# Kernel tuning notes

Measured on AMD Instinct MI355X. Metric: run time of the kernel, lower is better.

The kernel has to match this reference:

```python
import jax, jax.numpy as jnp
import numpy as np

NUM_USERS = 50000
NUM_ITEMS = 50000
LATENT_DIM = 64
NUM_INTERACTIONS = 1600000
N_LAYERS = 4  # 4 ODE blocks, euler 1-step each == 4 LightGCN propagations


def setup_inputs() -> dict:
    key = jax.random.key(0)
    k1, k2, k3, k4, k5 = jax.random.split(key, 5)
    user_emb = 0.1 * jax.random.normal(k1, (NUM_USERS, LATENT_DIM), dtype=jnp.float32)
    item_emb = 0.1 * jax.random.normal(k2, (NUM_ITEMS, LATENT_DIM), dtype=jnp.float32)
    eu = jax.random.randint(k3, (NUM_INTERACTIONS,), 0, NUM_USERS, dtype=jnp.int32)
    ei = jax.random.randint(jax.random.fold_in(k3, 1), (NUM_INTERACTIONS,), 0, NUM_ITEMS, dtype=jnp.int32)
    edge_index = jnp.stack([eu, ei])  # [2, E] user->item interactions
    users = jax.random.randint(k4, (4096,), 0, NUM_USERS, dtype=jnp.int32)
    items = jax.random.randint(k5, (4096,), 0, NUM_ITEMS, dtype=jnp.int32)
    return {"user_emb": user_emb, "item_emb": item_emb,
            "edge_index": edge_index, "users": users, "items": items}


def _graph(edge_index):
    # Symmetric bipartite graph over n_users + n_items nodes, normalized D^-1/2 A D^-1/2.
    eu, ei = edge_index[0], edge_index[1] + NUM_USERS
    rows = jnp.concatenate([eu, ei])
    cols = jnp.concatenate([ei, eu])
    n = NUM_USERS + NUM_ITEMS
    deg = jax.ops.segment_sum(jnp.ones_like(rows, dtype=jnp.float32), rows, num_segments=n)
    dinv = jnp.where(deg > 0, jax.lax.rsqrt(jnp.maximum(deg, 1.0)), 0.0)
    w = dinv[rows] * dinv[cols]  # [2E]
    return rows, cols, w


def _propagate(x, rows, cols, w):
    # sparse matmul: out[r] += w_e * x[c]  (irregular gather + segment-sum)
    n = NUM_USERS + NUM_ITEMS
    return jax.ops.segment_sum(x[cols] * w[:, None], rows, num_segments=n)


def _computer(user_emb, item_emb, edge_index):
    rows, cols, w = _graph(edge_index)
    e0 = jnp.concatenate([user_emb, item_emb])  # [N, d]
    # fixed-time euler: block_k(x) = x + A x; residual subtraction leaves A x
    embs = [e0]
    x = e0
    for _ in range(N_LAYERS):
        x = _propagate(x, rows, cols, w)
        embs.append(x)
    light_out = jnp.mean(jnp.stack(embs, axis=1), axis=1)  # [N, d]
    return light_out[:NUM_USERS], light_out[NUM_USERS:]


def reference(user_emb, item_emb, edge_index, users, items):
    all_users, all_items = _computer(user_emb, item_emb, edge_index)
    u = all_users[users]
    i = all_items[items]
    gamma = jnp.sum(u * i, axis=1)  # [B]
    return gamma
```

## Files before the change

kernel.cpp:

```cpp
#include <hip/hip_runtime.h>

#define LAT 64
#define ELLC 64
#define RB 256
#define RBSH 8
#define MAXBUK 512
#define RPT 8

#define SC0 64.0f
#define RSC 3.0f

typedef float f32x2 __attribute__((ext_vector_type(2)));

__global__ void __launch_bounds__(1024)
bin_k(const int* __restrict__ eu, const int* __restrict__ ei,
      int* __restrict__ gcur, unsigned int* __restrict__ bbuf,
      int2* __restrict__ ovf, int* __restrict__ ovfc,
      int E, int U, int nbuk, int cap, int ovf_cap) {
    __shared__ int lcnt[MAXBUK];
    __shared__ int lbase[MAXBUK];
    for (int i = threadIdx.x; i < nbuk; i += blockDim.x) lcnt[i] = 0;
    __syncthreads();
    int tid = blockIdx.x * blockDim.x + threadIdx.x;
    int stride = gridDim.x * blockDim.x;
    int ru[RPT], rc[RPT];
    int ne = 0;
#pragma unroll
    for (int k = 0; k < RPT; ++k) {
        int d = tid + k * stride;
        if (d < E) {
            int u = eu[d], c = ei[d] + U;
            ru[k] = u; rc[k] = c; ne = k + 1;
            atomicAdd(&lcnt[u >> RBSH], 1);
            atomicAdd(&lcnt[c >> RBSH], 1);
        }
    }
    __syncthreads();
    for (int b = threadIdx.x; b < nbuk; b += blockDim.x)
        lbase[b] = atomicAdd(&gcur[b], lcnt[b]);
    __syncthreads();
#pragma unroll
    for (int k = 0; k < RPT; ++k) {
        if (k < ne) {
            int u = ru[k], c = rc[k];
            int b = u >> RBSH;
            int pos = atomicAdd(&lbase[b], 1);
            if (pos < cap)
                bbuf[(size_t)b * cap + pos] = ((unsigned)(u & (RB - 1)) << 17) | (unsigned)c;
            else { int o = atomicAdd(ovfc, 1); if (o < ovf_cap) ovf[o] = make_int2(u, c); }
            b = c >> RBSH;
            pos = atomicAdd(&lbase[b], 1);
            if (pos < cap)
                bbuf[(size_t)b * cap + pos] = ((unsigned)(c & (RB - 1)) << 17) | (unsigned)u;
            else { int o = atomicAdd(ovfc, 1); if (o < ovf_cap) ovf[o] = make_int2(c, u); }
        }
    }
}

__global__ void __launch_bounds__(1024)
build_k(const unsigned int* __restrict__ bbuf, const int* __restrict__ gcur,
        int* __restrict__ cnt, int* __restrict__ colE, float* __restrict__ dinv,
        const float* __restrict__ ue, const float* __restrict__ ie,
        unsigned char* __restrict__ y0,
        int2* __restrict__ rovf, int* __restrict__ rovfc,
        int N, int U, int cap, int rovf_cap) {
    __shared__ int lcnt[RB];
    __shared__ float ldv[RB];
    int b = blockIdx.x;
    for (int i = threadIdx.x; i < RB; i += blockDim.x) lcnt[i] = 0;
    __syncthreads();
    int nb = min(gcur[b], cap);
    const unsigned int* src = bbuf + (size_t)b * cap;
    for (int e = threadIdx.x; e < nb; e += blockDim.x) {
        unsigned w = src[e];
        int r7 = (int)(w >> 17);
        int c = (int)(w & 0x1FFFF);
        int pos = atomicAdd(&lcnt[r7], 1);
        int r = (b << RBSH) + r7;
        if (pos < ELLC) colE[(size_t)r * ELLC + pos] = c;
        else { int o = atomicAdd(rovfc, 1); if (o < rovf_cap) rovf[o] = make_int2(r, c); }
    }
    __syncthreads();
    for (int i = threadIdx.x; i < RB; i += blockDim.x) {
        int r = (b << RBSH) + i;
        if (r < N) {
            int d = lcnt[i];
            cnt[r] = d;
            float dv = (d > 0) ? rsqrtf((float)d) : 0.0f;
            dinv[r] = dv;
            ldv[i] = dv;
        }
    }
    __syncthreads();
    int r0 = b << RBSH;
    int rows = min(RB, N - r0);
    for (int w = threadIdx.x; w < rows * ELLC; w += blockDim.x) {
        int i = w >> 6, pos = w & 63;
        if (pos >= lcnt[i]) colE[(size_t)(r0 + i) * ELLC + pos] = 0;
    }
    for (int w = threadIdx.x; w < rows * 16; w += blockDim.x) {
        int i = w >> 4, j = w & 15;
        int r = r0 + i;
        const float* s = (r < U) ? (ue + (size_t)r * LAT) : (ie + (size_t)(r - U) * LAT);
        float4 f = ((const float4*)s)[j];
        float sc = SC0 * ldv[i];
        int p = __builtin_amdgcn_cvt_pk_fp8_f32(sc * f.x, sc * f.y, 0, false);
        p = __builtin_amdgcn_cvt_pk_fp8_f32(sc * f.z, sc * f.w, p, true);
        ((unsigned*)y0)[(size_t)r * 16 + j] = (unsigned)p;
    }
}

__global__ void __launch_bounds__(1024)
fix_k(const int2* __restrict__ ovf, const int* __restrict__ ovfc,
      int* __restrict__ cnt, int* __restrict__ colE, float* __restrict__ dinv,
      const float* __restrict__ ue, const float* __restrict__ ie,
      unsigned char* __restrict__ y0,
      int2* __restrict__ rovf, int* __restrict__ rovfc,
      int ovf_cap, int rovf_cap, int U) {
    int n = min(*ovfc, ovf_cap);
    for (int i = threadIdx.x; i < n; i += blockDim.x) {
        int r = ovf[i].x, c = ovf[i].y;
        int pos = atomicAdd(&cnt[r], 1);
        if (pos < ELLC) colE[(size_t)r * ELLC + pos] = c;
        else { int o = atomicAdd(rovfc, 1); if (o < rovf_cap) rovf[o] = make_int2(r, c); }
    }
    __syncthreads();
    for (int i = threadIdx.x; i < n; i += blockDim.x) {
        int r = ovf[i].x;
        int d = cnt[r];
        dinv[r] = (d > 0) ? rsqrtf((float)d) : 0.0f;
    }
    __syncthreads();
    for (int w = threadIdx.x; w < n * 16; w += blockDim.x) {
        int o = w >> 4, j = w & 15;
        int r = ovf[o].x;
        const float* s = (r < U) ? (ue + (size_t)r * LAT) : (ie + (size_t)(r - U) * LAT);
        float4 f = ((const float4*)s)[j];
        float sc = SC0 * dinv[r];
        int p = __builtin_amdgcn_cvt_pk_fp8_f32(sc * f.x, sc * f.y, 0, false);
        p = __builtin_amdgcn_cvt_pk_fp8_f32(sc * f.z, sc * f.w, p, true);
        ((unsigned*)y0)[(size_t)r * 16 + j] = (unsigned)p;
    }
}

__device__ __forceinline__ void acc_word(unsigned w, float* r) {
    f32x2 lo = __builtin_amdgcn_cvt_pk_f32_fp8((int)w, false);
    f32x2 hi = __builtin_amdgcn_cvt_pk_f32_fp8((int)w, true);
    r[0] += lo[0]; r[1] += lo[1]; r[2] += hi[0]; r[3] += hi[1];
}

__global__ void __launch_bounds__(256, 4)
prop_h_k(const int* __restrict__ cnt, const int* __restrict__ colE,
         const float* __restrict__ dinv, const unsigned char* __restrict__ yin,
         unsigned char* __restrict__ yout,
         const int* __restrict__ users, const int* __restrict__ items,
         float* __restrict__ qacc,
         const float* __restrict__ ue, const float* __restrict__ ie,
         const int2* __restrict__ rovf, const int* __restrict__ rovfc,
         int rovf_cap, int B, int U, int first, int N, float inv_sin) {
    int wave = blockIdx.x * (blockDim.x >> 6) + (threadIdx.x >> 6);
    int lane = threadIdx.x & 63;
    int NW = (N + 3) >> 2;
    if (wave >= NW) {
        int qw = wave - NW;
        if (qw >= 2 * B) return;
        int node = (qw < B) ? users[qw] : (items[qw - B] + U);
        if (first) {
            float v = (node < U) ? ue[(size_t)node * LAT + lane]
                                 : ie[(size_t)(node - U) * LAT + lane];
            qacc[qw * LAT + lane] = v;
        } else {
            float di = dinv[node];
            unsigned bb = yin[(size_t)node * LAT + lane];
            f32x2 yv = __builtin_amdgcn_cvt_pk_f32_fp8((int)bb, false);
            qacc[qw * LAT + lane] += (di > 0.0f) ? yv[0] * inv_sin / di : 0.0f;
        }
        return;
    }
    int grp  = lane >> 4;
    int gbase = lane & 48;
    int q  = (lane >> 2) & 3;
    int s4 = lane & 3;
    int node = (wave << 2) + grp;
    int nadr = min(node, N - 1);
    int len = (node < N) ? min(cnt[nadr], ELLC) : 0;
    const int* cp = colE + (size_t)nadr * ELLC;
    int gl = lane & 15;
    int ca0 = cp[gl], ca1 = cp[16 + gl], ca2 = cp[32 + gl], ca3 = cp[48 + gl];
    int wmax = len;
    wmax = max(wmax, __shfl_xor(wmax, 16));
    wmax = max(wmax, __shfl_xor(wmax, 32));
    wmax = __builtin_amdgcn_readfirstlane(wmax);
    const uint4* y16 = (const uint4*)yin;

    float r[16];
#pragma unroll
    for (int j = 0; j < 16; ++j) r[j] = 0.f;

#pragma unroll
    for (int c = 0; c < 4; ++c) {
        int cac = (c == 0) ? ca0 : (c == 1) ? ca1 : (c == 2) ? ca2 : ca3;
#pragma unroll
        for (int si = 0; si < 4; ++si) {
            int s = (c << 2) + si;
            if ((s << 2) < wmax) {
                int col = __shfl(cac, gbase + (si << 2) + q);
                if ((s << 2) + q < len) {
                    uint4 v = y16[(size_t)col * 4 + s4];
                    acc_word(v.x, r + 0); acc_word(v.y, r + 4);
                    acc_word(v.z, r + 8); acc_word(v.w, r + 12);
                }
            }
        }
    }
    int novf = min(*rovfc, rovf_cap);
    for (int o = 0; o < novf; ++o) {
        int2 eo = rovf[o];
        if (eo.x == node && q == 0) {
            uint4 vv = y16[(size_t)eo.y * 4 + s4];
            acc_word(vv.x, r + 0); acc_word(vv.y, r + 4);
            acc_word(vv.z, r + 8); acc_word(vv.w, r + 12);
        }
    }
    {
        bool hi = (lane & 4) != 0;
        float s8[8], k8[8];
#pragma unroll
        for (int i = 0; i < 8; ++i) { k8[i] = hi ? r[8 + i] : r[i]; s8[i] = hi ? r[i] : r[8 + i]; }
#pragma unroll
        for (int i = 0; i < 8; ++i) r[i] = k8[i] + __shfl_xor(s8[i], 4);
    }
    {
        bool hi = (lane & 8) != 0;
        float s4a[4], k4a[4];
#pragma unroll
        for (int i = 0; i < 4; ++i) { k4a[i] = hi ? r[4 + i] : r[i]; s4a[i] = hi ? r[i] : r[4 + i]; }
#pragma unroll
        for (int i = 0; i < 4; ++i) r[i] = k4a[i] + __shfl_xor(s4a[i], 8);
    }
    float dv = dinv[nadr];
    float f = dv * dv * RSC;
    int pk = __builtin_amdgcn_cvt_pk_fp8_f32(f * r[0], f * r[1], 0, false);
    pk = __builtin_amdgcn_cvt_pk_fp8_f32(f * r[2], f * r[3], pk, true);
    if (node < N) {
        int b2 = (lane >> 2) & 1, b3 = (lane >> 3) & 1;
        ((unsigned*)yout)[(size_t)node * 16 + (s4 << 2) + (b2 << 1) + b3] = (unsigned)pk;
    }
}

__global__ void final_k(const float* __restrict__ qacc, const unsigned char* __restrict__ y4,
                        const float* __restrict__ dinv,
                        const int* __restrict__ users, const int* __restrict__ items,
                        float* __restrict__ out, int B, int U, float inv_s4) {
    int wave = blockIdx.x * (blockDim.x >> 6) + (threadIdx.x >> 6);
    int lane = threadIdx.x & 63;
    if (wave >= B) return;
    int un = users[wave];
    int in = items[wave] + U;
    float du = dinv[un], di = dinv[in];
    unsigned bu = y4[(size_t)un * LAT + lane];
    unsigned bi = y4[(size_t)in * LAT + lane];
    f32x2 xuv = __builtin_amdgcn_cvt_pk_f32_fp8((int)bu, false);
    f32x2 xiv = __builtin_amdgcn_cvt_pk_f32_fp8((int)bi, false);
    float au = qacc[wave * LAT + lane]       + ((du > 0.f) ? xuv[0] * inv_s4 / du : 0.f);
    float ai = qacc[(wave + B) * LAT + lane] + ((di > 0.f) ? xiv[0] * inv_s4 / di : 0.f);
    float p = au * ai;
#pragma unroll
    for (int off = 32; off > 0; off >>= 1) p += __shfl_down(p, off);
    if (lane == 0) out[wave] = p * (1.0f / 25.0f);
}

extern "C" void kernel_launch(void* const* d_in, const int* in_sizes, int n_in,
                              void* d_out, int out_size, void* d_ws, size_t ws_size,
                              hipStream_t stream) {
    const float* ue = (const float*)d_in[0];
    const float* ie = (const float*)d_in[1];
    const int* edge = (const int*)d_in[2];
    const int* users = (const int*)d_in[3];
    const int* items = (const int*)d_in[4];

    const int U = in_sizes[0] / LAT;
    const int I = in_sizes[1] / LAT;
    const int N = U + I;
    const int E = in_sizes[2] / 2;
    const int B = in_sizes[3];
    const int* eu = edge;
    const int* ei = edge + E;

    const int nbuk = (N + RB - 1) / RB;
    const int cap = ((2 * E / nbuk) * 5 / 4 + 255) & ~255;

    char* ws = (char*)d_ws;
    size_t off = 0;
    auto alloc = [&](size_t bytes) -> void* {
        void* p = ws + off;
        off += (bytes + 255) & ~(size_t)255;
        return p;
    };
    int*           cnt  = (int*)alloc((size_t)4 * N);
    float*         dinv = (float*)alloc((size_t)4 * N);
    int*           colE = (int*)alloc((size_t)4 * N * ELLC);
    unsigned char* yA   = (unsigned char*)alloc((size_t)N * LAT);
    unsigned char* yB   = (unsigned char*)alloc((size_t)N * LAT);
    float*         qacc = (float*)alloc((size_t)4 * 2 * B * LAT);
    unsigned*      bbuf = (unsigned*)alloc((size_t)4 * nbuk * cap);
    size_t zoff = off;
    int*      gcur = (int*)alloc((size_t)4 * nbuk);
    int*      ovfc = (int*)alloc(256);
    size_t zbytes = off - zoff;
    size_t remain = (ws_size > off + 256) ? (ws_size - off - 256) : 0;
    int ovf_cap = (int)min((size_t)131072, remain / (2 * sizeof(int2)));
    int2* ovf  = (int2*)alloc((size_t)ovf_cap * sizeof(int2));
    int2* rovf = (int2*)alloc((size_t)ovf_cap * sizeof(int2));
    int* rovfc = ovfc + 64;

    hipError_t _e = hipMemsetAsync(gcur, 0, zbytes, stream); (void)_e;

    const int tb = 256;

    bin_k<<<256, 1024, 0, stream>>>(eu, ei, gcur, bbuf, ovf, ovfc, E, U, nbuk, cap, ovf_cap);
    build_k<<<nbuk, 1024, 0, stream>>>(bbuf, gcur, cnt, colE, dinv, ue, ie, yA,
                                       rovf, rovfc, N, U, cap, ovf_cap);
    fix_k<<<1, 1024, 0, stream>>>(ovf, ovfc, cnt, colE, dinv, ue, ie, yA,
                                  rovf, rovfc, ovf_cap, ovf_cap, U);

    const int wpb = tb / 64;
    const int NW = (N + 3) >> 2;
    int pgrid = (NW + 2 * B + wpb - 1) / wpb;

    unsigned char* yin = yA;
    unsigned char* yout = yB;
    float s_in = SC0;
    for (int layer = 0; layer < 4; ++layer) {
        prop_h_k<<<pgrid, tb, 0, stream>>>(cnt, colE, dinv, yin, yout,
                                           users, items, qacc, ue, ie, rovf, rovfc,
                                           ovf_cap, B, U, layer == 0 ? 1 : 0, N,
                                           1.0f / s_in);
        s_in *= RSC;
        unsigned char* tmp = yin; yin = yout; yout = tmp;
    }

    final_k<<<(B + wpb - 1) / wpb, tb, 0, stream>>>(qacc, yin, dinv, users, items,
                                                    (float*)d_out, B, U, 1.0f / s_in);
}
```

Measured before the change: 255.3 us.

## Replace two-pass bucketed ELL build with direct global-atomic scatter

Replaces the bin/build/fix three-kernel graph construction (LDS-bucketed binning into a staging buffer, then per-bucket ELL fill) with a single kernel that scatters each edge straight into the ELL column array using global atomics on per-row counters. A separate per-row kernel then computes dinv, zero-pads unused ELL slots and writes the scaled fp8 initial embeddings. This removes the staging buffer round trip and one launch, but relies on 3.2M contended global atomics with random row targets and scattered 4-byte writes, which may cost more than the coalesced, LDS-based binning it replaces.

```diff
diff --git a/kernel.cpp b/kernel.cpp
--- a/kernel.cpp
+++ b/kernel.cpp
@@ -2,144 +2,48 @@
 
 #define LAT 64
 #define ELLC 64
-#define RB 256
-#define RBSH 8
-#define MAXBUK 512
-#define RPT 8
 
 #define SC0 64.0f
 #define RSC 3.0f
 
 typedef float f32x2 __attribute__((ext_vector_type(2)));
 
-__global__ void __launch_bounds__(1024)
-bin_k(const int* __restrict__ eu, const int* __restrict__ ei,
-      int* __restrict__ gcur, unsigned int* __restrict__ bbuf,
-      int2* __restrict__ ovf, int* __restrict__ ovfc,
-      int E, int U, int nbuk, int cap, int ovf_cap) {
-    __shared__ int lcnt[MAXBUK];
-    __shared__ int lbase[MAXBUK];
-    for (int i = threadIdx.x; i < nbuk; i += blockDim.x) lcnt[i] = 0;
-    __syncthreads();
+__global__ void __launch_bounds__(256)
+ell_k(const int* __restrict__ eu, const int* __restrict__ ei,
+      int* __restrict__ cnt, int* __restrict__ colE,
+      int2* __restrict__ rovf, int* __restrict__ rovfc,
+      int E, int U, int rovf_cap) {
     int tid = blockIdx.x * blockDim.x + threadIdx.x;
     int stride = gridDim.x * blockDim.x;
-    int ru[RPT], rc[RPT];
-    int ne = 0;
-#pragma unroll
-    for (int k = 0; k < RPT; ++k) {
-        int d = tid + k * stride;
-        if (d < E) {
-            int u = eu[d], c = ei[d] + U;
-            ru[k] = u; rc[k] = c; ne = k + 1;
-            atomicAdd(&lcnt[u >> RBSH], 1);
-            atomicAdd(&lcnt[c >> RBSH], 1);
-        }
-    }
-    __syncthreads();
-    for (int b = threadIdx.x; b < nbuk; b += blockDim.x)
-        lbase[b] = atomicAdd(&gcur[b], lcnt[b]);
-    __syncthreads();
-#pragma unroll
-    for (int k = 0; k < RPT; ++k) {
-        if (k < ne) {
-            int u = ru[k], c = rc[k];
-            int b = u >> RBSH;
-            int pos = atomicAdd(&lbase[b], 1);
-            if (pos < cap)
-                bbuf[(size_t)b * cap + pos] = ((unsigned)(u & (RB - 1)) << 17) | (unsigned)c;
-            else { int o = atomicAdd(ovfc, 1); if (o < ovf_cap) ovf[o] = make_int2(u, c); }
-            b = c >> RBSH;
-            pos = atomicAdd(&lbase[b], 1);
-            if (pos < cap)
-                bbuf[(size_t)b * cap + pos] = ((unsigned)(c & (RB - 1)) << 17) | (unsigned)u;
-            else { int o = atomicAdd(ovfc, 1); if (o < ovf_cap) ovf[o] = make_int2(c, u); }
-        }
-    }
-}
-
-__global__ void __launch_bounds__(1024)
-build_k(const unsigned int* __restrict__ bbuf, const int* __restrict__ gcur,
-        int* __restrict__ cnt, int* __restrict__ colE, float* __restrict__ dinv,
-        const float* __restrict__ ue, const float* __restrict__ ie,
-        unsigned char* __restrict__ y0,
-        int2* __restrict__ rovf, int* __restrict__ rovfc,
-        int N, int U, int cap, int rovf_cap) {
-    __shared__ int lcnt[RB];
-    __shared__ float ldv[RB];
-    int b = blockIdx.x;
-    for (int i = threadIdx.x; i < RB; i += blockDim.x) lcnt[i] = 0;
-    __syncthreads();
-    int nb = min(gcur[b], cap);
-    const unsigned int* src = bbuf + (size_t)b * cap;
-    for (int e = threadIdx.x; e < nb; e += blockDim.x) {
-        unsigned w = src[e];
-        int r7 = (int)(w >> 17);
-        int c = (int)(w & 0x1FFFF);
-        int pos = atomicAdd(&lcnt[r7], 1);
-        int r = (b << RBSH) + r7;
-        if (pos < ELLC) colE[(size_t)r * ELLC + pos] = c;
-        else { int o = atomicAdd(rovfc, 1); if (o < rovf_cap) rovf[o] = make_int2(r, c); }
-    }
-    __syncthreads();
-    for (int i = threadIdx.x; i < RB; i += blockDim.x) {
-        int r = (b << RBSH) + i;
-        if (r < N) {
-            int d = lcnt[i];
-            cnt[r] = d;
-            float dv = (d > 0) ? rsqrtf((float)d) : 0.0f;
-            dinv[r] = dv;
-            ldv[i] = dv;
-        }
-    }
-    __syncthreads();
-    int r0 = b << RBSH;
-    int rows = min(RB, N - r0);
-    for (int w = threadIdx.x; w < rows * ELLC; w += blockDim.x) {
-        int i = w >> 6, pos = w & 63;
-        if (pos >= lcnt[i]) colE[(size_t)(r0 + i) * ELLC + pos] = 0;
-    }
-    for (int w = threadIdx.x; w < rows * 16; w += blockDim.x) {
-        int i = w >> 4, j = w & 15;
-        int r = r0 + i;
+    for (int d = tid; d < E; d += stride) {
+        int u = eu[d], c = ei[d] + U;
+        int pos = atomicAdd(&cnt[u], 1);
+        if (pos < ELLC) colE[(size_t)u * ELLC + pos] = c;
+        else { int o = atomicAdd(rovfc, 1); if (o < rovf_cap) rovf[o] = make_int2(u, c); }
+        pos = atomicAdd(&cnt[c], 1);
+        if (pos < ELLC) colE[(size_t)c * ELLC + pos] = u;
+        else { int o = atomicAdd(rovfc, 1); if (o < rovf_cap) rovf[o] = make_int2(c, u); }
+    }
+}
+
+__global__ void __launch_bounds__(256)
+y0_k(const int* __restrict__ cnt, int* __restrict__ colE, float* __restrict__ dinv,
+     const float* __restrict__ ue, const float* __restrict__ ie,
+     unsigned char* __restrict__ y0, int N, int U) {
+    int r = blockIdx.x * (blockDim.x >> 6) + (threadIdx.x >> 6);
+    int lane = threadIdx.x & 63;
+    if (r >= N) return;
+    int d = cnt[r];
+    if (lane >= min(d, ELLC)) colE[(size_t)r * ELLC + lane] = 0;
+    float dv = (d > 0) ? rsqrtf((float)d) : 0.0f;
+    if (lane == 0) dinv[r] = dv;
+    if (lane < 16) {
         const float* s = (r < U) ? (ue + (size_t)r * LAT) : (ie + (size_t)(r - U) * LAT);
-        float4 f = ((const float4*)s)[j];
-        float sc = SC0 * ldv[i];
+        float4 f = ((const float4*)s)[lane];
+        float sc = SC0 * dv;
         int p = __builtin_amdgcn_cvt_pk_fp8_f32(sc * f.x, sc * f.y, 0, false);
         p = __builtin_amdgcn_cvt_pk_fp8_f32(sc * f.z, sc * f.w, p, true);
-        ((unsigned*)y0)[(size_t)r * 16 + j] = (unsigned)p;
-    }
-}
-
-__global__ void __launch_bounds__(1024)
-fix_k(const int2* __restrict__ ovf, const int* __restrict__ ovfc,
-      int* __restrict__ cnt, int* __restrict__ colE, float* __restrict__ dinv,
-      const float* __restrict__ ue, const float* __restrict__ ie,
-      unsigned char* __restrict__ y0,
-      int2* __restrict__ rovf, int* __restrict__ rovfc,
-      int ovf_cap, int rovf_cap, int U) {
-    int n = min(*ovfc, ovf_cap);
-    for (int i = threadIdx.x; i < n; i += blockDim.x) {
-        int r = ovf[i].x, c = ovf[i].y;
-        int pos = atomicAdd(&cnt[r], 1);
-        if (pos < ELLC) colE[(size_t)r * ELLC + pos] = c;
-        else { int o = atomicAdd(rovfc, 1); if (o < rovf_cap) rovf[o] = make_int2(r, c); }
-    }
-    __syncthreads();
-    for (int i = threadIdx.x; i < n; i += blockDim.x) {
-        int r = ovf[i].x;
-        int d = cnt[r];
-        dinv[r] = (d > 0) ? rsqrtf((float)d) : 0.0f;
-    }
-    __syncthreads();
-    for (int w = threadIdx.x; w < n * 16; w += blockDim.x) {
-        int o = w >> 4, j = w & 15;
-        int r = ovf[o].x;
-        const float* s = (r < U) ? (ue + (size_t)r * LAT) : (ie + (size_t)(r - U) * LAT);
-        float4 f = ((const float4*)s)[j];
-        float sc = SC0 * dinv[r];
-        int p = __builtin_amdgcn_cvt_pk_fp8_f32(sc * f.x, sc * f.y, 0, false);
-        p = __builtin_amdgcn_cvt_pk_fp8_f32(sc * f.z, sc * f.w, p, true);
-        ((unsigned*)y0)[(size_t)r * 16 + j] = (unsigned)p;
+        ((unsigned*)y0)[(size_t)r * 16 + lane] = (unsigned)p;
     }
 }
 
@@ -287,9 +191,6 @@
     const int* eu = edge;
     const int* ei = edge + E;
 
-    const int nbuk = (N + RB - 1) / RB;
-    const int cap = ((2 * E / nbuk) * 5 / 4 + 255) & ~255;
-
     char* ws = (char*)d_ws;
     size_t off = 0;
     auto alloc = [&](size_t bytes) -> void* {
@@ -297,32 +198,25 @@
         off += (bytes + 255) & ~(size_t)255;
         return p;
     };
-    int*           cnt  = (int*)alloc((size_t)4 * N);
+    size_t zoff = off;
+    int*           cnt   = (int*)alloc((size_t)4 * N);
+    int*           rovfc = (int*)alloc(256);
+    size_t zbytes = off - zoff;
     float*         dinv = (float*)alloc((size_t)4 * N);
     int*           colE = (int*)alloc((size_t)4 * N * ELLC);
     unsigned char* yA   = (unsigned char*)alloc((size_t)N * LAT);
     unsigned char* yB   = (unsigned char*)alloc((size_t)N * LAT);
     float*         qacc = (float*)alloc((size_t)4 * 2 * B * LAT);
-    unsigned*      bbuf = (unsigned*)alloc((size_t)4 * nbuk * cap);
-    size_t zoff = off;
-    int*      gcur = (int*)alloc((size_t)4 * nbuk);
-    int*      ovfc = (int*)alloc(256);
-    size_t zbytes = off - zoff;
     size_t remain = (ws_size > off + 256) ? (ws_size - off - 256) : 0;
-    int ovf_cap = (int)min((size_t)131072, remain / (2 * sizeof(int2)));
-    int2* ovf  = (int2*)alloc((size_t)ovf_cap * sizeof(int2));
-    int2* rovf = (int2*)alloc((size_t)ovf_cap * sizeof(int2));
-    int* rovfc = ovfc + 64;
-
-    hipError_t _e = hipMemsetAsync(gcur, 0, zbytes, stream); (void)_e;
+    int rovf_cap = (int)min((size_t)131072, remain / sizeof(int2));
+    int2* rovf = (int2*)alloc((size_t)rovf_cap * sizeof(int2));
+
+    hipError_t _e = hipMemsetAsync(cnt, 0, zbytes, stream); (void)_e;
 
     const int tb = 256;
 
-    bin_k<<<256, 1024, 0, stream>>>(eu, ei, gcur, bbuf, ovf, ovfc, E, U, nbuk, cap, ovf_cap);
-    build_k<<<nbuk, 1024, 0, stream>>>(bbuf, gcur, cnt, colE, dinv, ue, ie, yA,
-                                       rovf, rovfc, N, U, cap, ovf_cap);
-    fix_k<<<1, 1024, 0, stream>>>(ovf, ovfc, cnt, colE, dinv, ue, ie, yA,
-                                  rovf, rovfc, ovf_cap, ovf_cap, U);
+    ell_k<<<2048, tb, 0, stream>>>(eu, ei, cnt, colE, rovf, rovfc, E, U, rovf_cap);
+    y0_k<<<(N + 3) / 4, tb, 0, stream>>>(cnt, colE, dinv, ue, ie, yA, N, U);
 
     const int wpb = tb / 64;
     const int NW = (N + 3) >> 2;
@@ -334,7 +228,7 @@
     for (int layer = 0; layer < 4; ++layer) {
         prop_h_k<<<pgrid, tb, 0, stream>>>(cnt, colE, dinv, yin, yout,
                                            users, items, qacc, ue, ie, rovf, rovfc,
-                                           ovf_cap, B, U, layer == 0 ? 1 : 0, N,
+                                           rovf_cap, B, U, layer == 0 ? 1 : 0, N,
                                            1.0f / s_in);
         s_in *= RSC;
         unsigned char* tmp = yin; yin = yout; yout = tmp;
```

New measurement: 499.6 us. 1.96x slower.
